# Kernel tuning notes

Hardware: AMD Instinct MI355X
Metric: run time of the kernel (lower is better)

The kernel has to match this reference:

```python
import jax, jax.numpy as jnp
import numpy as np

B, D, H, O = 32, 128, 256, 10


def setup_inputs() -> dict:
    key = jax.random.key(0)
    ks = jax.random.split(key, 8)
    return {
        "t": jax.random.uniform(ks[0], (1,), dtype=jnp.float32),
        "state_batch": jax.random.normal(ks[1], (2 * B, D), dtype=jnp.float32),
        "x0": jax.random.normal(ks[2], (B, D), dtype=jnp.float32),
        "x1": jax.random.normal(ks[3], (B, D), dtype=jnp.float32),
        "W1": jax.random.normal(ks[4], (D, H), dtype=jnp.float32) / np.sqrt(D),
        "b1": jax.random.normal(ks[5], (H,), dtype=jnp.float32) * 0.01,
        "W2": jax.random.normal(ks[6], (H, O), dtype=jnp.float32) / np.sqrt(H),
        "b2": jax.random.normal(ks[7], (O,), dtype=jnp.float32) * 0.01,
    }


def reference(t, state_batch, x0, x1, W1, b1, W2, b2):
    b = x0.shape[0]
    deviation, dev_velocity = state_batch[:b], state_batch[b:]  # [B,D] each
    tt = t[0]
    window = 4.0 * tt * (1.0 - tt)
    # point on the perturbed path
    x = x0 + tt * (x1 - x0) + window * deviation  # [B,D]

    def f_single(xs):  # [D] -> [O]
        return jnp.tanh(xs @ W1 + b1) @ W2 + b2

    def G_single(xs):  # [D] -> [D,D] pullback metric J^T J + eps I
        J = jax.jacrev(f_single)(xs)  # [O,D] (O small -> reverse mode)
        return J.T @ J + 1e-4 * jnp.eye(xs.shape[0], dtype=xs.dtype)

    # dG[b,i,j,k] = d G_ij / d x_k  -- replaces the torch double autograd loop
    dG = jax.vmap(jax.jacfwd(G_single))(x)  # [B,D,D,D]
    dG = dG / (jnp.sqrt(jnp.sum(dG * dG, axis=(1, 2, 3), keepdims=True)) + 1e-6)
    # Christoffel symbols (first kind, up to normalization as in source)
    Gamma = 0.5 * (dG + jnp.transpose(dG, (0, 2, 1, 3)) - jnp.transpose(dG, (0, 3, 1, 2)))
    a = -jnp.einsum('bijk,bj,bk->bi', Gamma, dev_velocity, dev_velocity)
    a = a / (jnp.linalg.norm(dev_velocity, axis=1, keepdims=True) + 1e-6)
    restoration = -0.1 * deviation
    return jnp.concatenate([dev_velocity, a + restoration], axis=0)  # [2B,D]
```

## Files before the change

kernel.cpp:

```cpp
#include <hip/hip_runtime.h>
#include <hip/hip_bf16.h>


#define NB 32
#define OP 0

__device__ int g_pdone = 0;
__device__ int g_bdone = 0;

template<int BF> __device__ __forceinline__ float ld(const void* p, int i) {
  if constexpr (BF) return __bfloat162float(((const __hip_bfloat16*)p)[i]);
  else return ((const float*)p)[i];
}
template<int BF> __device__ __forceinline__ void st(void* p, int i, float v) {
  if constexpr (BF) ((__hip_bfloat16*)p)[i] = __float2bfloat16(v);
  else ((float*)p)[i] = v;
}
__device__ __forceinline__ float b2f(unsigned short u) {
  return __uint_as_float(((unsigned int)u) << 16);
}
template<int BF> __device__ __forceinline__ void ld8v(const void* p, int i, float* o) {
  if constexpr (BF) {
    uint4 u = *(const uint4*)((const unsigned short*)p + i);
    o[0] = b2f((unsigned short)(u.x & 0xffff)); o[1] = b2f((unsigned short)(u.x >> 16));
    o[2] = b2f((unsigned short)(u.y & 0xffff)); o[3] = b2f((unsigned short)(u.y >> 16));
    o[4] = b2f((unsigned short)(u.z & 0xffff)); o[5] = b2f((unsigned short)(u.z >> 16));
    o[6] = b2f((unsigned short)(u.w & 0xffff)); o[7] = b2f((unsigned short)(u.w >> 16));
  } else {
    float4 a = *(const float4*)((const float*)p + i);
    float4 b = *(const float4*)((const float*)p + i + 4);
    o[0]=a.x; o[1]=a.y; o[2]=a.z; o[3]=a.w; o[4]=b.x; o[5]=b.y; o[6]=b.z; o[7]=b.w;
  }
}

__device__ __forceinline__ int blocksniff(const void* sb, int* sh) {
  if (threadIdx.x == 0) *sh = 0;
  __syncthreads();
  float v = fabsf(__bfloat162float(((const __hip_bfloat16*)sb)[threadIdx.x & 255]));
  if (!(v < 1000.0f)) atomicOr(sh, 1);
  __syncthreads();
  return (*sh == 0) ? 1 : 0;
}

#define LXS   0
#define LVS   128
#define LW2   256
#define LYS   2816
#define LRED  2832
#define LHW   2928
#define LF1   3440
#define LEL   4976
#define LSW2  8048
#define LCL   11120
#define LCQ   11220
#define LW2P  11520
#define LTOT  14592

#define F1ACC(wv, gidx) do { \
    const float* sp_ = &sm[LSW2 + (gidx)*12]; \
    float4 s0_ = *(const float4*)sp_; \
    float4 s1_ = *(const float4*)(sp_+4); \
    float2 s2_ = *(const float2*)(sp_+8); \
    fa[0]+=(wv)*s0_.x; fa[1]+=(wv)*s0_.y; fa[2]+=(wv)*s0_.z; fa[3]+=(wv)*s0_.w; \
    fa[4]+=(wv)*s1_.x; fa[5]+=(wv)*s1_.y; fa[6]+=(wv)*s1_.z; fa[7]+=(wv)*s1_.w; \
    fa[8]+=(wv)*s2_.x; fa[9]+=(wv)*s2_.y; \
  } while (0)

template<int BF>
__device__ void fk_body(const void* tin, const void* sbin, const void* x0in,
                        const void* x1in, const void* W1in, const void* b1in,
                        const void* W2in, void* out, float* ws, float* sm) {
  int bid = blockIdx.x, t = threadIdx.x;
  if (bid >= NB) {
    int row0 = (bid - NB) * 2;
    float* colh = sm;
    if (t < 256) {
      int qq = t >> 7, d = t & 127;
      colh[qq * 128 + d] = ld<BF>(W1in, d * 256 + row0 + qq);
    }
    __syncthreads();
    int q = t >> 8, c = t & 255;
    const float* ch = &colh[q * 128];
    float pacc = 0.f;
    for (int d = 0; d < 128; d += 4) {
      float4 c4 = *(const float4*)&ch[d];
      pacc += c4.x * ld<BF>(W1in, (d + 0) * 256 + c);
      pacc += c4.y * ld<BF>(W1in, (d + 1) * 256 + c);
      pacc += c4.z * ld<BF>(W1in, (d + 2) * 256 + c);
      pacc += c4.w * ld<BF>(W1in, (d + 3) * 256 + c);
    }
    __hip_atomic_store(&ws[OP + (row0 + q) * 256 + c], pacc,
                       __ATOMIC_RELAXED, __HIP_MEMORY_SCOPE_AGENT);
    __syncthreads();
    if (t == 0)
      __hip_atomic_fetch_add(&g_pdone, 1, __ATOMIC_RELAXED, __HIP_MEMORY_SCOPE_AGENT);
    return;
  }
  int b = bid;
  int t2 = t & 255;
  int q  = t >> 8;
  int w  = t >> 6;
  int r  = t & 127;
  int qr = t >> 7;
  float tt = ld<BF>(tin, 0);
  float window = 4.f * tt * (1.f - tt);
  if (t < 128) {
    float dev = ld<BF>(sbin, b * 128 + t);
    float v   = ld<BF>(sbin, (NB + b) * 128 + t);
    float x0v = ld<BF>(x0in, b * 128 + t);
    float x1v = ld<BF>(x1in, b * 128 + t);
    sm[LXS + t] = x0v + tt * (x1v - x0v) + window * dev;
    sm[LVS + t] = v;
  }
  for (int i = t; i < 2560; i += 512) sm[LW2 + i] = ld<BF>(W2in, i);
  __syncthreads();
  float hp = q ? 0.f : ld<BF>(b1in, t2), wp = 0.f;
  {
    int d0 = q * 64;
    for (int d = d0; d < d0 + 64; d += 4) {
      float4 xv = *(const float4*)&sm[LXS + d];
      float4 vv = *(const float4*)&sm[LVS + d];
      float w0 = ld<BF>(W1in, (d + 0) * 256 + t2);
      float w1 = ld<BF>(W1in, (d + 1) * 256 + t2);
      float w2 = ld<BF>(W1in, (d + 2) * 256 + t2);
      float w3 = ld<BF>(W1in, (d + 3) * 256 + t2);
      hp += w0 * xv.x + w1 * xv.y + w2 * xv.z + w3 * xv.w;
      wp += w0 * vv.x + w1 * vv.y + w2 * vv.z + w3 * vv.w;
    }
  }
  if (q) { sm[LHW + t2 * 2] = hp; sm[LHW + t2 * 2 + 1] = wp; }
  float w2r[10];
  #pragma unroll
  for (int o = 0; o < 10; ++o) w2r[o] = sm[LW2 + t2 * 10 + o];
  __syncthreads();
  float ug = 0.f;
  if (!q) {
    float hacc = hp + sm[LHW + t2 * 2];
    float wacc = wp + sm[LHW + t2 * 2 + 1];
    float z  = tanhf(hacc);
    float sg = 1.f - z * z;
    ug = -2.f * z * sg;
    #pragma unroll
    for (int o = 0; o < 10; ++o) sm[LSW2 + t2 * 12 + o] = sg * w2r[o];
    float cval = ug * wacc * wacc;
    float rv[11];
    #pragma unroll
    for (int o = 0; o < 10; ++o) rv[o] = cval * w2r[o];
    rv[10] = (t < 128) ? sm[LVS + t] * sm[LVS + t] : 0.f;
    #pragma unroll
    for (int o = 0; o < 11; ++o) {
      float v = rv[o];
      #pragma unroll
      for (int m = 32; m > 0; m >>= 1) v += __shfl_xor(v, m);
      if ((t & 63) == 0) sm[LRED + w * 12 + o] = v;
    }
  }
  __syncthreads();
  if (t < 11) {
    float s = sm[LRED + t] + sm[LRED + 12 + t] + sm[LRED + 24 + t] + sm[LRED + 36 + t];
    if (t < 10) sm[LYS + t] = s;
    else        sm[LYS + 10] = sqrtf(s);
  }
  float fa[10];
  #pragma unroll
  for (int o = 0; o < 10; ++o) fa[o] = 0.f;
  {
    int gbase = qr * 64;
    for (int gg = 0; gg < 64; gg += 8) {
      int g = gbase + gg;
      float wv[8];
      ld8v<BF>(W1in, r * 256 + g, wv);
      F1ACC(wv[0], g + 0); F1ACC(wv[1], g + 1);
      F1ACC(wv[2], g + 2); F1ACC(wv[3], g + 3);
      F1ACC(wv[4], g + 4); F1ACC(wv[5], g + 5);
      F1ACC(wv[6], g + 6); F1ACC(wv[7], g + 7);
    }
  }
  if (qr == 1) {
    #pragma unroll
    for (int o = 0; o < 10; ++o) sm[LEL + r * 12 + o] = fa[o];
  } else if (qr == 2) {
    #pragma unroll
    for (int o = 0; o < 10; ++o) sm[LEL + 1536 + r * 12 + o] = fa[o];
  } else if (qr == 3) {
    #pragma unroll
    for (int o = 0; o < 10; ++o) sm[LW2P + r * 12 + o] = fa[o];
  }
  __syncthreads();
  float aun = 0.f;
  if (!qr) {
    #pragma unroll
    for (int o = 0; o < 10; ++o) {
      float f = fa[o] + sm[LEL + r * 12 + o] + sm[LEL + 1536 + r * 12 + o]
                      + sm[LW2P + r * 12 + o];
      sm[LF1 + r * 12 + o] = f;
      aun += f * sm[LYS + o];
    }
  }
  __syncthreads();
  float er[10];
  #pragma unroll
  for (int o = 0; o < 10; ++o) er[o] = 0.f;
  {
    int d0 = q * 64;
    for (int d = d0; d < d0 + 64; ++d) {
      float w1v = ld<BF>(W1in, d * 256 + t2);
      const float* fp = &sm[LF1 + d * 12];
      float4 a0 = *(const float4*)fp;
      float4 a1 = *(const float4*)(fp + 4);
      float2 a2 = *(const float2*)(fp + 8);
      er[0] += w1v * a0.x; er[1] += w1v * a0.y; er[2] += w1v * a0.z; er[3] += w1v * a0.w;
      er[4] += w1v * a1.x; er[5] += w1v * a1.y; er[6] += w1v * a1.z; er[7] += w1v * a1.w;
      er[8] += w1v * a2.x; er[9] += w1v * a2.y;
    }
  }
  if (q) {
    #pragma unroll
    for (int o = 0; o < 10; ++o) sm[LW2P + t2 * 12 + o] = er[o];
  }
  __syncthreads();
  if (!q) {
    #pragma unroll
    for (int o = 0; o < 10; ++o)
      sm[LEL + t2 * 12 + o] = er[o] + sm[LW2P + t2 * 12 + o];
    sm[LEL + t2 * 12 + 10] = ug;
    sm[LEL + t2 * 12 + 11] = 0.f;
  }
  __syncthreads();
  for (int i = t; i < 3072; i += 512) {
    int rr = i / 12, cc = i - rr * 12;
    sm[LW2P + i] = (cc < 10) ? sm[LW2 + rr * 10 + cc] : 0.f;
  }
  float cpart = 0.f;
  if (t < 400) {
    int chk = t / 100, idx = t - chk * 100;
    int o = idx / 10, p = idx - o * 10;
    const float* sa = &sm[LSW2 + o];
    const float* sb = &sm[LEL + p];
    int g0 = chk * 64;
    #pragma unroll 4
    for (int g = g0; g < g0 + 64; ++g) cpart += sa[g * 12] * sb[g * 12];
    if (chk) sm[LCQ + (chk - 1) * 100 + idx] = cpart;
  }
  __syncthreads();
  if (t < 100)
    sm[LCL + t] = cpart + sm[LCQ + t] + sm[LCQ + 100 + t] + sm[LCQ + 200 + t];
  __syncthreads();
  float cwr[10];
  #pragma unroll
  for (int o = 0; o < 10; ++o) {
    float cw = 0.f;
    #pragma unroll
    for (int p = 0; p < 10; ++p) cw += sm[LCL + o * 10 + p] * w2r[p];
    cwr[o] = cw;
  }
  float uc;
  {
    const float* ep = &sm[LEL + t2 * 12];
    float4 e0 = *(const float4*)ep;
    float4 e1 = *(const float4*)(ep + 4);
    float4 e2 = *(const float4*)(ep + 8);
    er[0]=e0.x; er[1]=e0.y; er[2]=e0.z; er[3]=e0.w;
    er[4]=e1.x; er[5]=e1.y; er[6]=e1.z; er[7]=e1.w;
    er[8]=e2.x; er[9]=e2.y; uc = e2.z;
  }
  if (t == 0) {
    while (__hip_atomic_load(&g_pdone, __ATOMIC_RELAXED, __HIP_MEMORY_SCOPE_AGENT) < 128)
      __builtin_amdgcn_s_sleep(2);
  }
  __syncthreads();
  int band = (t2 >> 6) * 64 + q * 32;
  float acc = 0.f;
  for (int i0 = 0; i0 < 32; i0 += 16) {
    float ph[16];
    #pragma unroll
    for (int j = 0; j < 16; ++j)
      ph[j] = ws[OP + (band + i0 + j) * 256 + t2];
    #pragma unroll
    for (int j = 0; j < 16; ++j) {
      int h = band + i0 + j;
      const float* rp = &sm[LEL + h * 12];
      float4 E0 = *(const float4*)rp;
      float4 E1 = *(const float4*)(rp + 4);
      float4 E2 = *(const float4*)(rp + 8);
      const float* wpp = &sm[LW2P + h * 12];
      float4 W0 = *(const float4*)wpp;
      float4 W1v = *(const float4*)(wpp + 4);
      float4 W2v = *(const float4*)(wpp + 8);
      float R = E0.x*w2r[0] + E0.y*w2r[1] + E0.z*w2r[2] + E0.w*w2r[3]
              + E1.x*w2r[4] + E1.y*w2r[5] + E1.z*w2r[6] + E1.w*w2r[7]
              + E2.x*w2r[8] + E2.y*w2r[9];
      float Rt = W0.x*er[0] + W0.y*er[1] + W0.z*er[2] + W0.w*er[3]
               + W1v.x*er[4] + W1v.y*er[5] + W1v.z*er[6] + W1v.w*er[7]
               + W2v.x*er[8] + W2v.y*er[9];
      float Qd = W0.x*cwr[0] + W0.y*cwr[1] + W0.z*cwr[2] + W0.w*cwr[3]
               + W1v.x*cwr[4] + W1v.y*cwr[5] + W1v.z*cwr[6] + W1v.w*cwr[7]
               + W2v.x*cwr[8] + W2v.y*cwr[9];
      acc += E2.z * ph[j] * (ph[j] * Qd + R * Rt);
    }
  }
  acc *= uc;
  #pragma unroll
  for (int m = 32; m > 0; m >>= 1) acc += __shfl_xor(acc, m);
  if ((t & 63) == 0) sm[LRED + w] = acc;
  __syncthreads();
  float F = sqrtf(fmaxf(2.f * (sm[LRED] + sm[LRED+1] + sm[LRED+2] + sm[LRED+3]
                             + sm[LRED+4] + sm[LRED+5] + sm[LRED+6] + sm[LRED+7]), 0.f));
  float denom = (F + 1e-6f) * (sm[LYS + 10] + 1e-6f);
  if (t < 128) {
    st<BF>(out, b * 128 + t, ld<BF>(sbin, (NB + b) * 128 + t));
    float dev = ld<BF>(sbin, b * 128 + t);
    float val = -aun / denom - 0.1f * dev;
    st<BF>(out, (NB + b) * 128 + t, val);
  }
  __syncthreads();
  if (t == 0) {
    int old = __hip_atomic_fetch_add(&g_bdone, 1, __ATOMIC_RELAXED, __HIP_MEMORY_SCOPE_AGENT);
    if (old == NB - 1) {
      __hip_atomic_store(&g_pdone, 0, __ATOMIC_RELAXED, __HIP_MEMORY_SCOPE_AGENT);
      __hip_atomic_store(&g_bdone, 0, __ATOMIC_RELAXED, __HIP_MEMORY_SCOPE_AGENT);
    }
  }
}

__global__ __launch_bounds__(512) void FK(const void* tin, const void* sbin,
                                          const void* x0in, const void* x1in,
                                          const void* W1in, const void* b1in,
                                          const void* W2in, void* out, float* ws) {
  __shared__ int sh;
  __shared__ __align__(16) float sm[LTOT];
  int bf = blocksniff(sbin, &sh);
  if (bf) fk_body<1>(tin, sbin, x0in, x1in, W1in, b1in, W2in, out, ws, sm);
  else    fk_body<0>(tin, sbin, x0in, x1in, W1in, b1in, W2in, out, ws, sm);
}

extern "C" void kernel_launch(void* const* d_in, const int* in_sizes, int n_in,
                              void* d_out, int out_size, void* d_ws, size_t ws_size,
                              hipStream_t stream) {
  float* ws = (float*)d_ws;
  const void* tin  = d_in[0];
  const void* sbin = d_in[1];
  const void* x0in = d_in[2];
  const void* x1in = d_in[3];
  const void* W1in = d_in[4];
  const void* b1in = d_in[5];
  const void* W2in = d_in[6];

  FK<<<dim3(NB + 128), dim3(512), 0, stream>>>(tin, sbin, x0in, x1in, W1in, b1in, W2in, d_out, ws);
}
```

Baseline: 91.25 us.

## Reuse precomputed W1 Gram matrix for E and aun, widen blocks to 1024 threads

```diff
diff --git a/kernel.cpp b/kernel.cpp
--- a/kernel.cpp
+++ b/kernel.cpp
@@ -3,6 +3,7 @@
 
 
 #define NB 32
+#define NH 64
 #define OP 0
 
 __device__ int g_pdone = 0;
@@ -47,24 +48,14 @@
 #define LW2   256
 #define LYS   2816
 #define LRED  2832
-#define LHW   2928
-#define LF1   3440
-#define LEL   4976
-#define LSW2  8048
-#define LCL   11120
-#define LCQ   11220
-#define LW2P  11520
-#define LTOT  14592
-
-#define F1ACC(wv, gidx) do { \
-    const float* sp_ = &sm[LSW2 + (gidx)*12]; \
-    float4 s0_ = *(const float4*)sp_; \
-    float4 s1_ = *(const float4*)(sp_+4); \
-    float2 s2_ = *(const float2*)(sp_+8); \
-    fa[0]+=(wv)*s0_.x; fa[1]+=(wv)*s0_.y; fa[2]+=(wv)*s0_.z; fa[3]+=(wv)*s0_.w; \
-    fa[4]+=(wv)*s1_.x; fa[5]+=(wv)*s1_.y; fa[6]+=(wv)*s1_.z; fa[7]+=(wv)*s1_.w; \
-    fa[8]+=(wv)*s2_.x; fa[9]+=(wv)*s2_.y; \
-  } while (0)
+#define LHW   3024
+#define LSW2  5072
+#define LEL   8144
+#define LW2P  11216
+#define LCL   14288
+#define LM    14400
+#define LAUN  14656
+#define LTOT  14784
 
 template<int BF>
 __device__ void fk_body(const void* tin, const void* sbin, const void* x0in,
@@ -72,15 +63,14 @@
                         const void* W2in, void* out, float* ws, float* sm) {
   int bid = blockIdx.x, t = threadIdx.x;
   if (bid >= NB) {
-    int row0 = (bid - NB) * 2;
-    float* colh = sm;
-    if (t < 256) {
+    int row0 = (bid - NB) * 4;
+    if (t < 512) {
       int qq = t >> 7, d = t & 127;
-      colh[qq * 128 + d] = ld<BF>(W1in, d * 256 + row0 + qq);
+      sm[qq * 128 + d] = ld<BF>(W1in, d * 256 + row0 + qq);
     }
     __syncthreads();
     int q = t >> 8, c = t & 255;
-    const float* ch = &colh[q * 128];
+    const float* ch = &sm[q * 128];
     float pacc = 0.f;
     for (int d = 0; d < 128; d += 4) {
       float4 c4 = *(const float4*)&ch[d];
@@ -97,11 +87,9 @@
     return;
   }
   int b = bid;
-  int t2 = t & 255;
-  int q  = t >> 8;
-  int w  = t >> 6;
-  int r  = t & 127;
-  int qr = t >> 7;
+  int t2  = t & 255;
+  int ch4 = t >> 8;
+  int w   = t >> 6;
   float tt = ld<BF>(tin, 0);
   float window = 4.f * tt * (1.f - tt);
   if (t < 128) {
@@ -111,13 +99,16 @@
     float x1v = ld<BF>(x1in, b * 128 + t);
     sm[LXS + t] = x0v + tt * (x1v - x0v) + window * dev;
     sm[LVS + t] = v;
-  }
-  for (int i = t; i < 2560; i += 512) sm[LW2 + i] = ld<BF>(W2in, i);
-  __syncthreads();
-  float hp = q ? 0.f : ld<BF>(b1in, t2), wp = 0.f;
-  {
-    int d0 = q * 64;
-    for (int d = d0; d < d0 + 64; d += 4) {
+    sm[LAUN + t] = 0.f;
+  }
+  for (int i = t; i < 2560; i += 1024) sm[LW2 + i] = ld<BF>(W2in, i);
+  for (int i = t; i < 3072; i += 1024) sm[LEL + i] = 0.f;
+  if (t < 100) sm[LCL + t] = 0.f;
+  __syncthreads();
+  float hp = (ch4 == 0) ? ld<BF>(b1in, t2) : 0.f, wp = 0.f;
+  {
+    int d0 = ch4 * 32;
+    for (int d = d0; d < d0 + 32; d += 4) {
       float4 xv = *(const float4*)&sm[LXS + d];
       float4 vv = *(const float4*)&sm[LVS + d];
       float w0 = ld<BF>(W1in, (d + 0) * 256 + t2);
@@ -128,15 +119,22 @@
       wp += w0 * vv.x + w1 * vv.y + w2 * vv.z + w3 * vv.w;
     }
   }
-  if (q) { sm[LHW + t2 * 2] = hp; sm[LHW + t2 * 2 + 1] = wp; }
+  sm[LHW + (ch4 * 256 + t2) * 2]     = hp;
+  sm[LHW + (ch4 * 256 + t2) * 2 + 1] = wp;
   float w2r[10];
   #pragma unroll
   for (int o = 0; o < 10; ++o) w2r[o] = sm[LW2 + t2 * 10 + o];
+  for (int i = t; i < 3072; i += 1024) {
+    int rr = i / 12, cc = i - rr * 12;
+    sm[LW2P + i] = (cc < 10) ? sm[LW2 + rr * 10 + cc] : 0.f;
+  }
   __syncthreads();
   float ug = 0.f;
-  if (!q) {
-    float hacc = hp + sm[LHW + t2 * 2];
-    float wacc = wp + sm[LHW + t2 * 2 + 1];
+  if (t < 256) {
+    float hacc = sm[LHW + t2 * 2]           + sm[LHW + (256 + t2) * 2]
+               + sm[LHW + (512 + t2) * 2]   + sm[LHW + (768 + t2) * 2];
+    float wacc = sm[LHW + t2 * 2 + 1]       + sm[LHW + (256 + t2) * 2 + 1]
+               + sm[LHW + (512 + t2) * 2 + 1] + sm[LHW + (768 + t2) * 2 + 1];
     float z  = tanhf(hacc);
     float sg = 1.f - z * z;
     ug = -2.f * z * sg;
@@ -161,92 +159,70 @@
     if (t < 10) sm[LYS + t] = s;
     else        sm[LYS + 10] = sqrtf(s);
   }
-  float fa[10];
-  #pragma unroll
-  for (int o = 0; o < 10; ++o) fa[o] = 0.f;
-  {
-    int gbase = qr * 64;
-    for (int gg = 0; gg < 64; gg += 8) {
-      int g = gbase + gg;
+  if (t == 0) {
+    while (__hip_atomic_load(&g_pdone, __ATOMIC_RELAXED, __HIP_MEMORY_SCOPE_AGENT) < NH)
+      __builtin_amdgcn_s_sleep(2);
+  }
+  __syncthreads();
+  if (t < 256) {
+    float m = 0.f;
+    #pragma unroll
+    for (int o = 0; o < 10; ++o) m += sm[LSW2 + t2 * 12 + o] * sm[LYS + o];
+    sm[LM + t2] = m;
+  }
+  {
+    float eacc[10];
+    #pragma unroll
+    for (int o = 0; o < 10; ++o) eacc[o] = 0.f;
+    int g0 = ch4 * 64;
+    for (int gg = 0; gg < 64; gg += 16) {
+      float ph[16];
+      #pragma unroll
+      for (int j = 0; j < 16; ++j)
+        ph[j] = ws[OP + (g0 + gg + j) * 256 + t2];
+      #pragma unroll
+      for (int j = 0; j < 16; ++j) {
+        const float* sp = &sm[LSW2 + (g0 + gg + j) * 12];
+        float4 s0 = *(const float4*)sp;
+        float4 s1 = *(const float4*)(sp + 4);
+        float2 s2 = *(const float2*)(sp + 8);
+        float p = ph[j];
+        eacc[0] += p * s0.x; eacc[1] += p * s0.y; eacc[2] += p * s0.z; eacc[3] += p * s0.w;
+        eacc[4] += p * s1.x; eacc[5] += p * s1.y; eacc[6] += p * s1.z; eacc[7] += p * s1.w;
+        eacc[8] += p * s2.x; eacc[9] += p * s2.y;
+      }
+    }
+    #pragma unroll
+    for (int o = 0; o < 10; ++o) atomicAdd(&sm[LEL + t2 * 12 + o], eacc[o]);
+  }
+  __syncthreads();
+  if (t < 256) sm[LEL + t2 * 12 + 10] = ug;
+  {
+    int r = t & 127, ch8 = t >> 7;
+    int ga0 = ch8 * 32;
+    float ap = 0.f;
+    for (int g = ga0; g < ga0 + 32; g += 8) {
       float wv[8];
       ld8v<BF>(W1in, r * 256 + g, wv);
-      F1ACC(wv[0], g + 0); F1ACC(wv[1], g + 1);
-      F1ACC(wv[2], g + 2); F1ACC(wv[3], g + 3);
-      F1ACC(wv[4], g + 4); F1ACC(wv[5], g + 5);
-      F1ACC(wv[6], g + 6); F1ACC(wv[7], g + 7);
-    }
-  }
-  if (qr == 1) {
-    #pragma unroll
-    for (int o = 0; o < 10; ++o) sm[LEL + r * 12 + o] = fa[o];
-  } else if (qr == 2) {
-    #pragma unroll
-    for (int o = 0; o < 10; ++o) sm[LEL + 1536 + r * 12 + o] = fa[o];
-  } else if (qr == 3) {
-    #pragma unroll
-    for (int o = 0; o < 10; ++o) sm[LW2P + r * 12 + o] = fa[o];
-  }
-  __syncthreads();
-  float aun = 0.f;
-  if (!qr) {
-    #pragma unroll
-    for (int o = 0; o < 10; ++o) {
-      float f = fa[o] + sm[LEL + r * 12 + o] + sm[LEL + 1536 + r * 12 + o]
-                      + sm[LW2P + r * 12 + o];
-      sm[LF1 + r * 12 + o] = f;
-      aun += f * sm[LYS + o];
-    }
-  }
-  __syncthreads();
-  float er[10];
-  #pragma unroll
-  for (int o = 0; o < 10; ++o) er[o] = 0.f;
-  {
-    int d0 = q * 64;
-    for (int d = d0; d < d0 + 64; ++d) {
-      float w1v = ld<BF>(W1in, d * 256 + t2);
-      const float* fp = &sm[LF1 + d * 12];
-      float4 a0 = *(const float4*)fp;
-      float4 a1 = *(const float4*)(fp + 4);
-      float2 a2 = *(const float2*)(fp + 8);
-      er[0] += w1v * a0.x; er[1] += w1v * a0.y; er[2] += w1v * a0.z; er[3] += w1v * a0.w;
-      er[4] += w1v * a1.x; er[5] += w1v * a1.y; er[6] += w1v * a1.z; er[7] += w1v * a1.w;
-      er[8] += w1v * a2.x; er[9] += w1v * a2.y;
-    }
-  }
-  if (q) {
-    #pragma unroll
-    for (int o = 0; o < 10; ++o) sm[LW2P + t2 * 12 + o] = er[o];
-  }
-  __syncthreads();
-  if (!q) {
-    #pragma unroll
-    for (int o = 0; o < 10; ++o)
-      sm[LEL + t2 * 12 + o] = er[o] + sm[LW2P + t2 * 12 + o];
-    sm[LEL + t2 * 12 + 10] = ug;
-    sm[LEL + t2 * 12 + 11] = 0.f;
-  }
-  __syncthreads();
-  for (int i = t; i < 3072; i += 512) {
-    int rr = i / 12, cc = i - rr * 12;
-    sm[LW2P + i] = (cc < 10) ? sm[LW2 + rr * 10 + cc] : 0.f;
-  }
-  float cpart = 0.f;
-  if (t < 400) {
+      ap += wv[0] * sm[LM + g]     + wv[1] * sm[LM + g + 1]
+          + wv[2] * sm[LM + g + 2] + wv[3] * sm[LM + g + 3]
+          + wv[4] * sm[LM + g + 4] + wv[5] * sm[LM + g + 5]
+          + wv[6] * sm[LM + g + 6] + wv[7] * sm[LM + g + 7];
+    }
+    atomicAdd(&sm[LAUN + r], ap);
+  }
+  if (t < 800) {
     int chk = t / 100, idx = t - chk * 100;
     int o = idx / 10, p = idx - o * 10;
-    const float* sa = &sm[LSW2 + o];
-    const float* sb = &sm[LEL + p];
-    int g0 = chk * 64;
+    int gc0 = chk * 32;
+    float cp = 0.f;
     #pragma unroll 4
-    for (int g = g0; g < g0 + 64; ++g) cpart += sa[g * 12] * sb[g * 12];
-    if (chk) sm[LCQ + (chk - 1) * 100 + idx] = cpart;
-  }
-  __syncthreads();
-  if (t < 100)
-    sm[LCL + t] = cpart + sm[LCQ + t] + sm[LCQ + 100 + t] + sm[LCQ + 200 + t];
-  __syncthreads();
-  float cwr[10];
+    for (int g = gc0; g < gc0 + 32; ++g)
+      cp += sm[LSW2 + g * 12 + o] * sm[LEL + g * 12 + p];
+    atomicAdd(&sm[LCL + idx], cp);
+  }
+  __syncthreads();
+  float cwr[10], er[10], uc;
   #pragma unroll
   for (int o = 0; o < 10; ++o) {
     float cw = 0.f;
@@ -254,7 +230,6 @@
     for (int p = 0; p < 10; ++p) cw += sm[LCL + o * 10 + p] * w2r[p];
     cwr[o] = cw;
   }
-  float uc;
   {
     const float* ep = &sm[LEL + t2 * 12];
     float4 e0 = *(const float4*)ep;
@@ -264,21 +239,16 @@
     er[4]=e1.x; er[5]=e1.y; er[6]=e1.z; er[7]=e1.w;
     er[8]=e2.x; er[9]=e2.y; uc = e2.z;
   }
-  if (t == 0) {
-    while (__hip_atomic_load(&g_pdone, __ATOMIC_RELAXED, __HIP_MEMORY_SCOPE_AGENT) < 128)
-      __builtin_amdgcn_s_sleep(2);
-  }
-  __syncthreads();
-  int band = (t2 >> 6) * 64 + q * 32;
+  int band = (t2 >> 6) * 64 + ch4 * 16;
   float acc = 0.f;
-  for (int i0 = 0; i0 < 32; i0 += 16) {
+  {
     float ph[16];
     #pragma unroll
     for (int j = 0; j < 16; ++j)
-      ph[j] = ws[OP + (band + i0 + j) * 256 + t2];
+      ph[j] = ws[OP + (band + j) * 256 + t2];
     #pragma unroll
     for (int j = 0; j < 16; ++j) {
-      int h = band + i0 + j;
+      int h = band + j;
       const float* rp = &sm[LEL + h * 12];
       float4 E0 = *(const float4*)rp;
       float4 E1 = *(const float4*)(rp + 4);
@@ -304,13 +274,15 @@
   for (int m = 32; m > 0; m >>= 1) acc += __shfl_xor(acc, m);
   if ((t & 63) == 0) sm[LRED + w] = acc;
   __syncthreads();
-  float F = sqrtf(fmaxf(2.f * (sm[LRED] + sm[LRED+1] + sm[LRED+2] + sm[LRED+3]
-                             + sm[LRED+4] + sm[LRED+5] + sm[LRED+6] + sm[LRED+7]), 0.f));
+  float fsum = 0.f;
+  #pragma unroll
+  for (int i = 0; i < 16; ++i) fsum += sm[LRED + i];
+  float F = sqrtf(fmaxf(2.f * fsum, 0.f));
   float denom = (F + 1e-6f) * (sm[LYS + 10] + 1e-6f);
   if (t < 128) {
     st<BF>(out, b * 128 + t, ld<BF>(sbin, (NB + b) * 128 + t));
     float dev = ld<BF>(sbin, b * 128 + t);
-    float val = -aun / denom - 0.1f * dev;
+    float val = -sm[LAUN + t] / denom - 0.1f * dev;
     st<BF>(out, (NB + b) * 128 + t, val);
   }
   __syncthreads();
@@ -323,10 +295,10 @@
   }
 }
 
-__global__ __launch_bounds__(512) void FK(const void* tin, const void* sbin,
-                                          const void* x0in, const void* x1in,
-                                          const void* W1in, const void* b1in,
-                                          const void* W2in, void* out, float* ws) {
+__global__ __launch_bounds__(1024) void FK(const void* tin, const void* sbin,
+                                           const void* x0in, const void* x1in,
+                                           const void* W1in, const void* b1in,
+                                           const void* W2in, void* out, float* ws) {
   __shared__ int sh;
   __shared__ __align__(16) float sm[LTOT];
   int bf = blocksniff(sbin, &sh);
@@ -346,5 +318,5 @@
   const void* b1in = d_in[5];
   const void* W2in = d_in[6];
 
-  FK<<<dim3(NB + 128), dim3(512), 0, stream>>>(tin, sbin, x0in, x1in, W1in, b1in, W2in, d_out, ws);
-}
+  FK<<<dim3(NB + NH), dim3(1024), 0, stream>>>(tin, sbin, x0in, x1in, W1in, b1in, W2in, d_out, ws);
+}
```

New measurement: 102.2 us. +12.0%, slower.
